# Kernel tuning notes

Measured on AMD Instinct MI355X. Metric: run time of the kernel, lower is better.

## Reference

```python
import math
import jax, jax.numpy as jnp
import numpy as np

B, T, D, V, S, R = 128, 32, 64, 4096, 32, 8
PONDER = 0.01
TWO_PI = np.float32(2.0 * math.pi)


def _ln(x, g, b, eps=1e-5):
    mu = x.mean(-1, keepdims=True)
    var = ((x - mu) ** 2).mean(-1, keepdims=True)
    return (x - mu) / jnp.sqrt(var + eps) * g + b


def _clin(xr, xi, Wr, br, Wi, bi):
    # ComplexLinear: fc_real/fc_imag share biases per torch module
    real = (xr @ Wr + br) - (xi @ Wi + bi)
    imag = (xi @ Wr + br) + (xr @ Wi + bi)
    return real, imag


def setup_inputs() -> dict:
    key = jax.random.key(0)
    ks = jax.random.split(key, 10)
    f = lambda k, sh, s: jax.random.normal(k, sh, jnp.float32) * s
    return {
        "x_seq": jax.random.randint(ks[0], (B, T), 0, V),
        "enc_emb": f(ks[1], (V, 2 * D), 0.02),
        "vq_emb": f(ks[2], (V, 2 * D), 0.05),
        "norm_rg": jnp.ones((D,), jnp.float32),
        "norm_rb": jnp.zeros((D,), jnp.float32),
        "norm_ig": jnp.ones((D,), jnp.float32),
        "norm_ib": jnp.zeros((D,), jnp.float32),
        "proj_w": f(ks[3], (3, 2, D, D), 0.05),  # [q/k/v, real/imag, in, out]
        "proj_b": f(ks[4], (3, 2, D), 0.01),
        "mem_gate_w": f(ks[5], (2 * D, 1), 0.05),
        "mem_gate_b": jnp.zeros((1,), jnp.float32),
        "arb_w": f(ks[6], (2 * D, 3), 0.05),
        "arb_b": jnp.zeros((3,), jnp.float32),
        "dec_w": f(ks[7], (2 * D, V), 0.02),
        "dec_b": jnp.zeros((V,), jnp.float32),
        "halt_bias": jnp.array(3.0, jnp.float32),
        "input_gate": jnp.array(0.0, jnp.float32),
    }


def _fwd(x_seq, enc_emb, vq_emb, norm_rg, norm_rb, norm_ig, norm_ib,
         proj_w, proj_b, mem_gate_w, mem_gate_b, arb_w, arb_b,
         dec_w, dec_b, halt_bias, input_gate):
    sg = jax.lax.stop_gradient
    emb = enc_emb[x_seq]                         # [B,T,2D]
    er, ei = emb[..., :D], emb[..., D:]
    alpha = jax.nn.sigmoid(input_gate)
    bias = jax.nn.softplus(halt_bias)
    vq_sq = (vq_emb ** 2).sum(-1)                # [V]

    def step(carry, xs):
        gw_r, gw_i, mem_r, mem_i = carry
        x_r, x_i = xs
        gw_r = alpha * gw_r + (1.0 - alpha) * x_r
        gw_i = alpha * gw_i + (1.0 - alpha) * x_i
        active = jnp.ones((x_r.shape[0],), jnp.float32)
        acc_vq = jnp.zeros_like(active)
        acc_ppx = jnp.zeros_like(active)
        acc_ent = jnp.zeros_like(active)
        acc_pond = jnp.zeros_like(active)
        acc_ph = jnp.zeros_like(active)
        prev_ang = jnp.arctan2(gw_i, gw_r)
        for _ in range(R):
            cr = _ln(gw_r, norm_rg, norm_rb)
            ci = _ln(gw_i, norm_ig, norm_ib)
            flat = jnp.concatenate([cr, ci], -1)            # [B,2D]
            # VQ (argmin over squared euclidean == argmin over cdist)
            d2 = (flat ** 2).sum(-1, keepdims=True) - 2.0 * (flat @ vq_emb.T) + vq_sq
            idx = jnp.argmin(d2, -1)                        # [B]
            zq = vq_emb[idx]                                # [B,2D]
            vq_loss = ((zq - sg(flat)) ** 2).mean(-1) + 0.25 * ((sg(zq) - flat) ** 2).mean(-1)
            zq_st = flat + sg(zq - flat)                    # straight-through
            avg = jax.nn.one_hot(idx, V, dtype=jnp.float32).mean(0)
            ent = -(avg * jnp.log(avg + 1e-10)).sum()
            ppx = jnp.exp(ent)
            vq_r, vq_i = zq_st[:, :D], zq_st[:, D:]
            # Hermitian gating
            qr, qi = _clin(cr, ci, proj_w[0, 0], proj_b[0, 0], proj_w[0, 1], proj_b[0, 1])
            kr, ki = _clin(cr, ci, proj_w[1, 0], proj_b[1, 0], proj_w[1, 1], proj_b[1, 1])
            wr, wi = _clin(cr, ci, proj_w[2, 0], proj_b[2, 0], proj_w[2, 1], proj_b[2, 1])
            gate = jax.nn.sigmoid((qr * kr + qi * ki).sum(-1, keepdims=True))
            g_r, g_i = wr * gate, wi * gate
            # memory read (mem unchanged during recursion)
            sim = jnp.einsum('bsd,bd->bs', mem_r, cr) + jnp.einsum('bsd,bd->bs', mem_i, ci)
            attn = jax.nn.softmax(sim, -1)
            m_r = jnp.einsum('bs,bsd->bd', attn, mem_r)
            m_i = jnp.einsum('bs,bsd->bd', attn, mem_i)
            # arbitrator mix
            gates = jax.nn.softmax(flat @ arb_w + arb_b, -1)  # [B,3]
            u_r = gates[:, 0:1] * g_r + gates[:, 1:2] * m_r + gates[:, 2:3] * vq_r
            u_i = gates[:, 0:1] * g_i + gates[:, 1:2] * m_i + gates[:, 2:3] * vq_i
            c_r = 0.6 * cr + 0.4 * u_r
            c_i = 0.6 * ci + 0.4 * u_i
            ang = jnp.arctan2(c_i, c_r)
            diff = jnp.abs(ang - prev_ang)
            diff = jnp.minimum(diff, TWO_PI - diff)
            acc_ph = acc_ph + active * diff.mean(-1)
            prev_ang = ang
            halt = jax.nn.sigmoid(bias - vq_loss)
            stop = (halt > 0.5).astype(jnp.float32)
            acc_pond = acc_pond + active * PONDER
            m = active > 0.5
            acc_vq = jnp.where(m, vq_loss, acc_vq)
            acc_ppx = jnp.where(m, ppx, acc_ppx)
            acc_ent = jnp.where(m, ent, acc_ent)
            gw_r = jnp.where(m[:, None], c_r, gw_r)
            gw_i = jnp.where(m[:, None], c_i, gw_i)
            active = active * (1.0 - stop)
        # final memory write (read output discarded, matching torch)
        flat_gw = jnp.concatenate([gw_r, gw_i], -1)
        wg = jax.nn.sigmoid(flat_gw @ mem_gate_w + mem_gate_b)  # [B,1]
        sh_r = jnp.roll(mem_r, 1, axis=1)
        sh_i = jnp.roll(mem_i, 1, axis=1)
        mem_r = sh_r.at[:, 0].set(wg * gw_r + (1.0 - wg) * sh_r[:, 0])
        mem_i = sh_i.at[:, 0].set(wg * gw_i + (1.0 - wg) * sh_i[:, 0])
        stats = jnp.stack([acc_vq.mean(), acc_ppx.mean(), acc_ent.mean(),
                           acc_pond.mean(), acc_ph.mean()])
        return (gw_r, gw_i, mem_r, mem_i), (gw_r, gw_i, stats)

    init = (jnp.zeros((B, D), jnp.float32), jnp.zeros((B, D), jnp.float32),
            jnp.zeros((B, S, D), jnp.float32), jnp.zeros((B, S, D), jnp.float32))
    xs = (jnp.moveaxis(er, 1, 0), jnp.moveaxis(ei, 1, 0))
    (gw_r, gw_i, mem_r, mem_i), (o_r, o_i, stats) = jax.lax.scan(step, init, xs)
    flat_out = jnp.concatenate([jnp.moveaxis(o_r, 0, 1), jnp.moveaxis(o_i, 0, 1)], -1)  # [B,T,2D]
    logits = flat_out @ dec_w + dec_b
    return logits, stats.mean(0), mem_r, mem_i


def reference(x_seq, enc_emb, vq_emb, norm_rg, norm_rb, norm_ig, norm_ib,
              proj_w, proj_b, mem_gate_w, mem_gate_b, arb_w, arb_b,
              dec_w, dec_b, halt_bias, input_gate):
    return _fwd(x_seq, enc_emb, vq_emb, norm_rg, norm_rb, norm_ig, norm_ib,
                proj_w, proj_b, mem_gate_w, mem_gate_b, arb_w, arb_b,
                dec_w, dec_b, halt_bias, input_gate)
```

## Files before the change

kernel.cpp:

```cpp
#include <hip/hip_runtime.h>
#include <math.h>

#define BB 128
#define TT 32
#define DDIM 64
#define VV 4096
#define SS 32
#define RR 8
#define NT 512
#define SMP 65

typedef unsigned short u16;
typedef unsigned int u32;
typedef _Float16 h2 __attribute__((ext_vector_type(2)));

__device__ __forceinline__ h2 bch(u32 u){ union { u32 u; h2 h; } v; v.u = u; return v.h; }

__device__ __forceinline__ float fdot2f(u32 a, u32 b, float acc){
#if __has_builtin(__builtin_amdgcn_fdot2)
  return __builtin_amdgcn_fdot2(bch(a), bch(b), acc, false);
#else
  h2 x = bch(a), y = bch(b);
  return acc + (float)x[0] * (float)y[0] + (float)x[1] * (float)y[1];
#endif
}

__device__ __forceinline__ u32 packh2(float a, float b){
  union { _Float16 h[2]; u32 u; } p;
  p.h[0] = (_Float16)a; p.h[1] = (_Float16)b;
  return p.u;
}

__device__ __forceinline__ void bar(){ __syncthreads(); }

__global__ __launch_bounds__(256) void k_pack(const float* __restrict__ vq, u32* __restrict__ vqT){
  int gid = blockIdx.x * 256 + threadIdx.x;
  int l   = gid & 63;
  int dc8 = (gid >> 6) & 15;
  int c0  = gid >> 10;
  int c   = (c0 << 6) + l;
  const float* s = vq + c * 128 + dc8 * 8;
  uint4 o;
  o.x = packh2(s[0], s[1]);
  o.y = packh2(s[2], s[3]);
  o.z = packh2(s[4], s[5]);
  o.w = packh2(s[6], s[7]);
  ((uint4*)vqT)[gid] = o;
}

__global__ __launch_bounds__(256) void k_vqsq(const float* __restrict__ vq, float* __restrict__ vqsq){
  int c = blockIdx.x * 256 + threadIdx.x;
  float s = 0.f;
  for (int d = 0; d < 128; d++){ float v = vq[c * 128 + d]; s = fmaf(v, v, s); }
  vqsq[c] = s;
}

__global__ __launch_bounds__(NT) void k_recur(
    const int* __restrict__ x_seq, const float* __restrict__ enc_emb,
    const float* __restrict__ vq_emb, const u32* __restrict__ vqT,
    const float* __restrict__ vq_sq,
    const float* __restrict__ nrg, const float* __restrict__ nrb,
    const float* __restrict__ nig, const float* __restrict__ nib,
    const float* __restrict__ proj_w, const float* __restrict__ proj_b,
    const float* __restrict__ mgw, const float* __restrict__ mgb,
    const float* __restrict__ arb_w, const float* __restrict__ arb_b,
    const float* __restrict__ hb, const float* __restrict__ ig,
    float* __restrict__ gwout,
    int* __restrict__ idxbuf, int* __restrict__ rstop_g, float* __restrict__ accs,
    float* __restrict__ out_mem)
{
  const int b = blockIdx.x;
  const int tid = threadIdx.x;
  const int lane = tid & 63;
  const int wave = tid >> 6;

  __shared__ __align__(16) float s_gw[128];
  __shared__ __align__(16) float s_flat[128];
  __shared__ __align__(16) u32   s_flath[64];
  __shared__ __align__(16) float s_c[128];
  __shared__ float s_mem[2][SS][SMP];
  __shared__ __align__(16) float s_qkw[6][DDIM];
  __shared__ float s_sim[SS];
  __shared__ float s_red[8];
  __shared__ float s_cand[8];
  __shared__ int   s_candi[8];

  for (int i = tid; i < 128; i += NT) s_gw[i] = 0.f;
  for (int i = tid; i < 2 * SS * SMP; i += NT) ((float*)s_mem)[i] = 0.f;
  __syncthreads();

  const float alpha = 1.f / (1.f + expf(-ig[0]));
  float bias_h; { float x = hb[0]; bias_h = log1pf(expf(x)); }
  int head = 0;
  float prev_ang = 0.f;

  #pragma unroll 1
  for (int t = 0; t < TT; t++){
    int xid = x_seq[b * TT + t];

    if (tid < 128){
      float e = enc_emb[xid * 128 + tid];
      s_gw[tid] = alpha * s_gw[tid] + (1.f - alpha) * e;
    }
    bar();
    if (wave == 0) prev_ang = atan2f(s_gw[64 + lane], s_gw[lane]);

    float acc_ph = 0.f, vl_last = 0.f;
    int rst = 0;
    bool stop = false;

    #pragma unroll 1
    for (int r = 0; r < RR; r++){
      if (wave < 2){
        float x = s_gw[wave * 64 + lane];
        float mu = x;
        #pragma unroll
        for (int m = 1; m < 64; m <<= 1) mu += __shfl_xor(mu, m);
        mu *= (1.f / 64.f);
        float dxl = x - mu;
        float vv = dxl * dxl;
        #pragma unroll
        for (int m = 1; m < 64; m <<= 1) vv += __shfl_xor(vv, m);
        vv *= (1.f / 64.f);
        float rs = 1.f / sqrtf(vv + 1e-5f);
        const float* g  = wave ? nig : nrg;
        const float* bb = wave ? nib : nrb;
        float fv = dxl * rs * g[lane] + bb[lane];
        s_flat[wave * 64 + lane] = fv;
        float pv = __shfl_xor(fv, 1);
        if ((lane & 1) == 0)
          s_flath[(wave * 64 + lane) >> 1] = packh2(fv, pv);
      }
      bar();

      uint4 F[16];
      {
        const uint4* sfh4 = (const uint4*)s_flath;
        #pragma unroll
        for (int i = 0; i < 16; i++) F[i] = sfh4[i];
      }
      float bsc = 3.4e38f; int bidx = 0;
      #pragma unroll 1
      for (int k = 0; k < 8; k++){
        int c0 = wave + 8 * k;
        const uint4* vp = ((const uint4*)vqT) + (c0 * 16) * 64 + lane;
        uint4 U[16];
        #pragma unroll
        for (int dc8 = 0; dc8 < 16; dc8++) U[dc8] = vp[dc8 * 64];
        float dot = 0.f;
        #pragma unroll
        for (int dc8 = 0; dc8 < 16; dc8++){
          dot = fdot2f(U[dc8].x, F[dc8].x, dot);
          dot = fdot2f(U[dc8].y, F[dc8].y, dot);
          dot = fdot2f(U[dc8].z, F[dc8].z, dot);
          dot = fdot2f(U[dc8].w, F[dc8].w, dot);
        }
        int c = c0 * 64 + lane;
        float sc = vq_sq[c] - 2.f * dot;
        if (sc < bsc || (sc == bsc && c < bidx)){ bsc = sc; bidx = c; }
      }
      #pragma unroll
      for (int m = 1; m < 64; m <<= 1){
        float os = __shfl_xor(bsc, m);
        int   oi = __shfl_xor(bidx, m);
        if (os < bsc || (os == bsc && oi < bidx)){ bsc = os; bidx = oi; }
      }
      if (lane == 0){ s_cand[wave] = bsc; s_candi[wave] = bidx; }
      bar();

      int imin = 0;
      if (wave < 2){
        float bs = s_cand[0]; int bi = s_candi[0];
        #pragma unroll
        for (int w = 1; w < 8; w++){
          float os = s_cand[w]; int oi = s_candi[w];
          if (os < bs || (os == bs && oi < bi)){ bs = os; bi = oi; }
        }
        imin = __builtin_amdgcn_readfirstlane(bi);
      }

      if (wave >= 2){
        const int w2 = wave - 2;
        const int p = w2 >> 1, ri = w2 & 1;
        const float* Wr = proj_w + ((p * 2 + 0) << 12);
        const float* Wi = proj_w + ((p * 2 + 1) << 12);
        const float* xA = s_flat + (ri ? 64 : 0);
        const float* xB = s_flat + (ri ? 0 : 64);
        float a0=0.f,a1=0.f,a2=0.f,a3=0.f, b0=0.f,b1=0.f,b2=0.f,b3=0.f;
        #pragma unroll
        for (int i = 0; i < 64; i += 4){
          float4 xv = *(const float4*)&xA[i];
          a0 = fmaf(xv.x, Wr[(i + 0) * 64 + lane], a0);
          a1 = fmaf(xv.y, Wr[(i + 1) * 64 + lane], a1);
          a2 = fmaf(xv.z, Wr[(i + 2) * 64 + lane], a2);
          a3 = fmaf(xv.w, Wr[(i + 3) * 64 + lane], a3);
        }
        #pragma unroll
        for (int i = 0; i < 64; i += 4){
          float4 xv = *(const float4*)&xB[i];
          b0 = fmaf(xv.x, Wi[(i + 0) * 64 + lane], b0);
          b1 = fmaf(xv.y, Wi[(i + 1) * 64 + lane], b1);
          b2 = fmaf(xv.z, Wi[(i + 2) * 64 + lane], b2);
          b3 = fmaf(xv.w, Wi[(i + 3) * 64 + lane], b3);
        }
        float A  = (a0 + a1) + (a2 + a3);
        float Bv = (b0 + b1) + (b2 + b3);
        float br  = proj_b[(p * 2 + 0) * 64 + lane];
        float bi2 = proj_b[(p * 2 + 1) * 64 + lane];
        s_qkw[w2][lane] = ri ? (A + Bv + br + bi2) : (A - Bv + br - bi2);
      } else if (wave == 0){
        const int s2 = lane & 31, h = lane >> 5;
        const float* mrow = &s_mem[h][s2][0];
        const float* fx = s_flat + h * 64;
        float a0=0.f,a1=0.f,a2=0.f,a3=0.f;
        #pragma unroll
        for (int d = 0; d < 64; d += 4){
          a0 = fmaf(mrow[d + 0], fx[d + 0], a0);
          a1 = fmaf(mrow[d + 1], fx[d + 1], a1);
          a2 = fmaf(mrow[d + 2], fx[d + 2], a2);
          a3 = fmaf(mrow[d + 3], fx[d + 3], a3);
        }
        float p = (a0 + a1) + (a2 + a3);
        p += __shfl_xor(p, 32);
        float mx = p;
        #pragma unroll
        for (int m = 1; m < 32; m <<= 1) mx = fmaxf(mx, __shfl_xor(mx, m));
        float e = expf(p - mx);
        float sm = e;
        #pragma unroll
        for (int m = 1; m < 32; m <<= 1) sm += __shfl_xor(sm, m);
        if (lane < 32) s_sim[lane] = e / sm;
      } else {
        float f0 = s_flat[lane], f1 = s_flat[64 + lane];
        float p0 = fmaf(f0, arb_w[lane * 3 + 0], f1 * arb_w[(64 + lane) * 3 + 0]);
        float p1 = fmaf(f0, arb_w[lane * 3 + 1], f1 * arb_w[(64 + lane) * 3 + 1]);
        float p2 = fmaf(f0, arb_w[lane * 3 + 2], f1 * arb_w[(64 + lane) * 3 + 2]);
        float z0 = vq_emb[imin * 128 + lane];
        float z1 = vq_emb[imin * 128 + 64 + lane];
        float d0 = z0 - f0, d1 = z1 - f1;
        float sq = d0 * d0 + d1 * d1;
        #pragma unroll
        for (int m = 1; m < 64; m <<= 1){
          p0 += __shfl_xor(p0, m); p1 += __shfl_xor(p1, m);
          p2 += __shfl_xor(p2, m); sq += __shfl_xor(sq, m);
        }
        if (lane == 0){
          s_red[4] = p0 + arb_b[0];
          s_red[5] = p1 + arb_b[1];
          s_red[6] = p2 + arb_b[2];
          s_red[0] = 1.25f * sq * (1.f / 128.f);
          idxbuf[(b * TT + t) * RR + r] = imin;
        }
      }
      bar();

      float vl = s_red[0];
      stop = (bias_h - vl) > 0.f;
      vl_last = vl; rst = r;

      if (tid < 128){
        float g = fmaf(s_qkw[0][lane], s_qkw[2][lane], s_qkw[1][lane] * s_qkw[3][lane]);
        #pragma unroll
        for (int m = 1; m < 64; m <<= 1) g += __shfl_xor(g, m);
        float gate = 1.f / (1.f + expf(-g));
        const int h = wave, j = lane;
        float m_reg = 0.f;
        #pragma unroll 8
        for (int s2 = 0; s2 < 32; s2++)
          m_reg = fmaf(s_sim[s2], s_mem[h][s2][j], m_reg);
        float l0 = s_red[4], l1 = s_red[5], l2 = s_red[6];
        float mx = fmaxf(l0, fmaxf(l1, l2));
        float e0 = expf(l0 - mx), e1 = expf(l1 - mx), e2 = expf(l2 - mx);
        float inv = 1.f / (e0 + e1 + e2);
        float zq = vq_emb[imin * 128 + tid];
        float wv = s_qkw[4 + h][j];
        float u = (e0 * inv) * (gate * wv) + (e1 * inv) * m_reg + (e2 * inv) * zq;
        float cv = 0.6f * s_flat[tid] + 0.4f * u;
        s_c[tid]  = cv;
        s_gw[tid] = cv;
      }
      bar();

      if (wave == 0){
        float ang = atan2f(s_c[64 + lane], s_c[lane]);
        float df = fabsf(ang - prev_ang);
        df = fminf(df, 6.28318530717958647692f - df);
        prev_ang = ang;
        #pragma unroll
        for (int m = 1; m < 64; m <<= 1) df += __shfl_xor(df, m);
        acc_ph += df * (1.f / 64.f);
      }
      if (stop) break;
    }

    float pond = 0.01f * (float)(rst + 1);
    if (tid < 128) gwout[(b * TT + t) * 128 + tid] = s_gw[tid];
    head = (head + SS - 1) & (SS - 1);
    if (wave < 2){
      float p = fmaf(s_c[lane], mgw[lane], s_c[64 + lane] * mgw[64 + lane]);
      #pragma unroll
      for (int m = 1; m < 64; m <<= 1) p += __shfl_xor(p, m);
      float wg = 1.f / (1.f + expf(-(p + mgb[0])));
      const int h = wave, d0 = lane;
      float old = s_mem[h][head][d0];
      s_mem[h][head][d0] = wg * s_c[h * 64 + d0] + (1.f - wg) * old;
    }
    if (tid == 0){
      int o = b * TT + t;
      rstop_g[o] = rst;
      accs[o * 4 + 0] = vl_last;
      accs[o * 4 + 1] = pond;
      accs[o * 4 + 2] = acc_ph;
    }
  }

  bar();
  for (int i = tid; i < SS * DDIM; i += NT){
    int s2 = i >> 6, d0 = i & 63;
    int ph = (head + s2) & (SS - 1);
    out_mem[b * SS * DDIM + i] = s_mem[0][ph][d0];
    out_mem[BB * SS * DDIM + b * SS * DDIM + i] = s_mem[1][ph][d0];
  }
}

__global__ void k_max(const int* __restrict__ rstop_g, int* __restrict__ maxr){
  int t = threadIdx.x;
  if (t >= TT) return;
  int mx = 0;
  for (int b = 0; b < BB; b++) mx = max(mx, rstop_g[b * TT + t]);
  maxr[t] = mx;
}

__global__ __launch_bounds__(256) void k_tail(
    const u32* __restrict__ vqT, const float* __restrict__ vq_sq,
    const float* __restrict__ gwout, const int* __restrict__ rstop_g,
    const int* __restrict__ maxr, int* __restrict__ idxbuf,
    const float* __restrict__ nrg, const float* __restrict__ nrb,
    const float* __restrict__ nig, const float* __restrict__ nib)
{
  int o = blockIdx.x;
  int t = o & (TT - 1);
  int rs = rstop_g[o];
  if (rs >= maxr[t]) return;
  __shared__ __align__(16) u32 sfh[64];
  __shared__ float s_cand[4];
  __shared__ int   s_candi[4];
  int tid = threadIdx.x, lane = tid & 63, wave = tid >> 6;
  if (wave < 2){
    float x = gwout[o * 128 + wave * 64 + lane];
    float mu = x;
    #pragma unroll
    for (int m = 1; m < 64; m <<= 1) mu += __shfl_xor(mu, m);
    mu *= (1.f / 64.f);
    float dxl = x - mu;
    float vv = dxl * dxl;
    #pragma unroll
    for (int m = 1; m < 64; m <<= 1) vv += __shfl_xor(vv, m);
    vv *= (1.f / 64.f);
    float rsn = 1.f / sqrtf(vv + 1e-5f);
    const float* g  = wave ? nig : nrg;
    const float* bb = wave ? nib : nrb;
    float fv = dxl * rsn * g[lane] + bb[lane];
    float pv = __shfl_xor(fv, 1);
    if ((lane & 1) == 0) sfh[(wave * 64 + lane) >> 1] = packh2(fv, pv);
  }
  __syncthreads();
  uint4 F[16];
  {
    const uint4* sfh4 = (const uint4*)sfh;
    #pragma unroll
    for (int i = 0; i < 16; i++) F[i] = sfh4[i];
  }
  float bsc = 3.4e38f; int bidx = 0;
  #pragma unroll 1
  for (int k = 0; k < 16; k++){
    int c0 = wave + 4 * k;
    const uint4* vp = ((const uint4*)vqT) + (c0 * 16) * 64 + lane;
    uint4 U[16];
    #pragma unroll
    for (int dc8 = 0; dc8 < 16; dc8++) U[dc8] = vp[dc8 * 64];
    float dot = 0.f;
    #pragma unroll
    for (int dc8 = 0; dc8 < 16; dc8++){
      dot = fdot2f(U[dc8].x, F[dc8].x, dot);
      dot = fdot2f(U[dc8].y, F[dc8].y, dot);
      dot = fdot2f(U[dc8].z, F[dc8].z, dot);
      dot = fdot2f(U[dc8].w, F[dc8].w, dot);
    }
    int c = c0 * 64 + lane;
    float sc = vq_sq[c] - 2.f * dot;
    if (sc < bsc || (sc == bsc && c < bidx)){ bsc = sc; bidx = c; }
  }
  #pragma unroll
  for (int m = 1; m < 64; m <<= 1){
    float os = __shfl_xor(bsc, m);
    int   oi = __shfl_xor(bidx, m);
    if (os < bsc || (os == bsc && oi < bidx)){ bsc = os; bidx = oi; }
  }
  if (lane == 0){ s_cand[wave] = bsc; s_candi[wave] = bidx; }
  __syncthreads();
  if (tid == 0){
    float bs = s_cand[0]; int bi = s_candi[0];
    for (int w = 1; w < 4; w++){
      float os = s_cand[w]; int oi = s_candi[w];
      if (os < bs || (os == bs && oi < bi)){ bs = os; bi = oi; }
    }
    for (int r = rs + 1; r < RR; r++) idxbuf[o * RR + r] = bi;
  }
}

__global__ __launch_bounds__(512) void k_stats(
    const int* __restrict__ idxbuf, const int* __restrict__ rstop_g,
    const float* __restrict__ accs, const int* __restrict__ maxr,
    float* __restrict__ out_stats)
{
  __shared__ float s_ent[TT][RR];
  __shared__ int   s_vals[8][128];
  __shared__ float s_fin[8][5];
  int tid = threadIdx.x, lane = tid & 63, wave = tid >> 6;

  for (int base = 0; base < TT * RR; base += 8){
    int p = base + wave;
    int r = p >> 5, t = p & 31;
    bool act = (r <= maxr[t]);
    s_vals[wave][lane]      = idxbuf[(lane * TT + t) * RR + r];
    s_vals[wave][64 + lane] = idxbuf[((64 + lane) * TT + t) * RR + r];
    __syncthreads();
    if (act){
      int mine1 = s_vals[wave][lane], mine2 = s_vals[wave][64 + lane];
      int c1 = 0, c2 = 0;
      for (int j = 0; j < 128; j++){
        int v = s_vals[wave][j];
        c1 += (v == mine1); c2 += (v == mine2);
      }
      float contrib = -(logf((float)c1 * (1.f / 128.f) + 1e-10f)
                      + logf((float)c2 * (1.f / 128.f) + 1e-10f)) * (1.f / 128.f);
      for (int m = 1; m < 64; m <<= 1) contrib += __shfl_xor(contrib, m);
      if (lane == 0) s_ent[t][r] = contrib;
    }
    __syncthreads();
  }

  float sv = 0.f, sp = 0.f, se = 0.f, sn = 0.f, sh = 0.f;
  for (int o = tid; o < BB * TT; o += 512){
    int t = o & 31;
    int rs = rstop_g[o];
    float ent = s_ent[t][rs];
    se += ent;
    sp += expf(ent);
    sv += accs[o * 4 + 0];
    sn += accs[o * 4 + 1];
    sh += accs[o * 4 + 2];
  }
  for (int m = 1; m < 64; m <<= 1){
    sv += __shfl_xor(sv, m); sp += __shfl_xor(sp, m); se += __shfl_xor(se, m);
    sn += __shfl_xor(sn, m); sh += __shfl_xor(sh, m);
  }
  if (lane == 0){
    s_fin[wave][0] = sv; s_fin[wave][1] = sp; s_fin[wave][2] = se;
    s_fin[wave][3] = sn; s_fin[wave][4] = sh;
  }
  __syncthreads();
  if (tid == 0){
    float a[5] = {0.f, 0.f, 0.f, 0.f, 0.f};
    for (int w = 0; w < 8; w++)
      for (int j = 0; j < 5; j++) a[j] += s_fin[w][j];
    float inv = 1.f / (float)(BB * TT);
    for (int j = 0; j < 5; j++) out_stats[j] = a[j] * inv;
  }
}

__global__ __launch_bounds__(256) void k_dec(
    const float* __restrict__ gwout, const float* __restrict__ dec_w,
    const float* __restrict__ dec_b, float* __restrict__ out)
{
  __shared__ float At[32][128];
  int tid = threadIdx.x;
  int row0 = blockIdx.y * 32;
  int col0 = blockIdx.x * 256;
  {
    const float4* src = (const float4*)(gwout + row0 * 128);
    float4* dst = (float4*)&At[0][0];
    for (int i = tid; i < 1024; i += 256) dst[i] = src[i];
  }
  __syncthreads();
  int v = col0 + tid;
  float acc[32];
  #pragma unroll
  for (int r2 = 0; r2 < 32; r2++) acc[r2] = 0.f;
  for (int k = 0; k < 128; k += 4){
    float w0 = dec_w[(k + 0) * 4096 + v];
    float w1 = dec_w[(k + 1) * 4096 + v];
    float w2 = dec_w[(k + 2) * 4096 + v];
    float w3 = dec_w[(k + 3) * 4096 + v];
    #pragma unroll
    for (int r2 = 0; r2 < 32; r2++){
      float4 a = *(const float4*)&At[r2][k];
      acc[r2] = fmaf(a.x, w0, fmaf(a.y, w1, fmaf(a.z, w2, fmaf(a.w, w3, acc[r2]))));
    }
  }
  float bv = dec_b[v];
  for (int r2 = 0; r2 < 32; r2++)
    out[(row0 + r2) * 4096 + v] = acc[r2] + bv;
}

extern "C" void kernel_launch(void* const* d_in, const int* in_sizes, int n_in,
                              void* d_out, int out_size, void* d_ws, size_t ws_size,
                              hipStream_t stream){
  const int*   x_seq   = (const int*)  d_in[0];
  const float* enc_emb = (const float*)d_in[1];
  const float* vq_emb  = (const float*)d_in[2];
  const float* nrg     = (const float*)d_in[3];
  const float* nrb     = (const float*)d_in[4];
  const float* nig     = (const float*)d_in[5];
  const float* nib     = (const float*)d_in[6];
  const float* proj_w  = (const float*)d_in[7];
  const float* proj_b  = (const float*)d_in[8];
  const float* mgw     = (const float*)d_in[9];
  const float* mgb     = (const float*)d_in[10];
  const float* arb_w   = (const float*)d_in[11];
  const float* arb_b   = (const float*)d_in[12];
  const float* dec_w   = (const float*)d_in[13];
  const float* dec_b   = (const float*)d_in[14];
  const float* hb      = (const float*)d_in[15];
  const float* ig      = (const float*)d_in[16];

  char* ws = (char*)d_ws;
  u32*   vqT    = (u32*)  (ws + 0);
  float* vqsq   = (float*)(ws + 2097152);
  float* gwout  = (float*)(ws + 2113536);
  int*   idxbuf = (int*)  (ws + 6307840);
  int*   rstop  = (int*)  (ws + 6438912);
  float* accs   = (float*)(ws + 6455296);
  int*   maxr   = (int*)  (ws + 6520832);

  float* out = (float*)d_out;
  float* out_stats = out + 16777216;
  float* out_mem   = out + 16777221;

  k_pack <<<dim3(256), dim3(256), 0, stream>>>(vq_emb, vqT);
  k_vqsq <<<dim3(16),  dim3(256), 0, stream>>>(vq_emb, vqsq);
  k_recur<<<dim3(BB),  dim3(NT),  0, stream>>>(
      x_seq, enc_emb, vq_emb, vqT, vqsq,
      nrg, nrb, nig, nib, proj_w, proj_b, mgw, mgb, arb_w, arb_b, hb, ig,
      gwout, idxbuf, rstop, accs, out_mem);
  k_dec  <<<dim3(16, 128), dim3(256), 0, stream>>>(gwout, dec_w, dec_b, out);
  k_max  <<<dim3(1),   dim3(64),  0, stream>>>(rstop, maxr);
  k_tail <<<dim3(BB * TT), dim3(256), 0, stream>>>(vqT, vqsq, gwout, rstop, maxr, idxbuf,
                                                   nrg, nrb, nig, nib);
  k_stats<<<dim3(1),   dim3(512), 0, stream>>>(idxbuf, rstop, accs, maxr, out_stats);
}
```

Measured before the change: 767.1 us.

## Restructure recurrence projection, prefetch embeddings, and parallelize stats across blocks

The recurrent kernel now prefetches the next token's embedding during the current step. The projection is changed so each wave multiplies one weight matrix against both the real and imaginary inputs, with biases and combination done later from shared memory. The argmin merge moves into the arbiter wave, the chosen codebook row is cached in shared memory, the VQ dot uses four independent accumulators, and the phase accumulation moves to wave 2. k_max uses more threads and zeroes the stats output, and k_stats runs one block per timestep, combining results with atomics instead of a single serial block. This removes serial tail work and latency, at the cost of float atomics that make the summation order nondeterministic.

```diff
diff --git a/kernel.cpp b/kernel.cpp
--- a/kernel.cpp
+++ b/kernel.cpp
@@ -78,8 +78,10 @@
   __shared__ __align__(16) float s_flat[128];
   __shared__ __align__(16) u32   s_flath[64];
   __shared__ __align__(16) float s_c[128];
+  __shared__ __align__(16) float s_zq[128];
+  __shared__ __align__(16) float s_enext[128];
   __shared__ float s_mem[2][SS][SMP];
-  __shared__ __align__(16) float s_qkw[6][DDIM];
+  __shared__ __align__(16) float s_mv[12][DDIM];
   __shared__ float s_sim[SS];
   __shared__ float s_red[8];
   __shared__ float s_cand[8];
@@ -87,25 +89,31 @@
 
   for (int i = tid; i < 128; i += NT) s_gw[i] = 0.f;
   for (int i = tid; i < 2 * SS * SMP; i += NT) ((float*)s_mem)[i] = 0.f;
+  if (tid < 128) s_enext[tid] = enc_emb[x_seq[b * TT] * 128 + tid];
   __syncthreads();
 
   const float alpha = 1.f / (1.f + expf(-ig[0]));
   float bias_h; { float x = hb[0]; bias_h = log1pf(expf(x)); }
   int head = 0;
   float prev_ang = 0.f;
+  float acc_ph = 0.f;
+
+  const float pb0r = proj_b[lane],        pb0i = proj_b[64 + lane];
+  const float pb1r = proj_b[128 + lane],  pb1i = proj_b[192 + lane];
+  const float pb2r = proj_b[256 + lane],  pb2i = proj_b[320 + lane];
+
+  const uint4* vqT4 = (const uint4*)vqT;
 
   #pragma unroll 1
   for (int t = 0; t < TT; t++){
-    int xid = x_seq[b * TT + t];
-
     if (tid < 128){
-      float e = enc_emb[xid * 128 + tid];
-      s_gw[tid] = alpha * s_gw[tid] + (1.f - alpha) * e;
+      s_gw[tid] = alpha * s_gw[tid] + (1.f - alpha) * s_enext[tid];
     }
     bar();
-    if (wave == 0) prev_ang = atan2f(s_gw[64 + lane], s_gw[lane]);
-
-    float acc_ph = 0.f, vl_last = 0.f;
+    if (wave == 2) prev_ang = atan2f(s_gw[64 + lane], s_gw[lane]);
+
+    float vl_last = 0.f;
+    if (wave == 2) acc_ph = 0.f;
     int rst = 0;
     bool stop = false;
 
@@ -143,20 +151,26 @@
       #pragma unroll 1
       for (int k = 0; k < 8; k++){
         int c0 = wave + 8 * k;
-        const uint4* vp = ((const uint4*)vqT) + (c0 * 16) * 64 + lane;
+        int c  = (c0 << 6) + lane;
+        float qv = vq_sq[c];
+        const uint4* vp = vqT4 + (c0 * 16) * 64 + lane;
         uint4 U[16];
         #pragma unroll
         for (int dc8 = 0; dc8 < 16; dc8++) U[dc8] = vp[dc8 * 64];
-        float dot = 0.f;
-        #pragma unroll
-        for (int dc8 = 0; dc8 < 16; dc8++){
-          dot = fdot2f(U[dc8].x, F[dc8].x, dot);
-          dot = fdot2f(U[dc8].y, F[dc8].y, dot);
-          dot = fdot2f(U[dc8].z, F[dc8].z, dot);
-          dot = fdot2f(U[dc8].w, F[dc8].w, dot);
-        }
-        int c = c0 * 64 + lane;
-        float sc = vq_sq[c] - 2.f * dot;
+        float a0 = 0.f, a1 = 0.f, a2 = 0.f, a3 = 0.f;
+        #pragma unroll
+        for (int dc8 = 0; dc8 < 16; dc8 += 4){
+          a0 = fdot2f(U[dc8+0].x, F[dc8+0].x, a0); a0 = fdot2f(U[dc8+0].y, F[dc8+0].y, a0);
+          a0 = fdot2f(U[dc8+0].z, F[dc8+0].z, a0); a0 = fdot2f(U[dc8+0].w, F[dc8+0].w, a0);
+          a1 = fdot2f(U[dc8+1].x, F[dc8+1].x, a1); a1 = fdot2f(U[dc8+1].y, F[dc8+1].y, a1);
+          a1 = fdot2f(U[dc8+1].z, F[dc8+1].z, a1); a1 = fdot2f(U[dc8+1].w, F[dc8+1].w, a1);
+          a2 = fdot2f(U[dc8+2].x, F[dc8+2].x, a2); a2 = fdot2f(U[dc8+2].y, F[dc8+2].y, a2);
+          a2 = fdot2f(U[dc8+2].z, F[dc8+2].z, a2); a2 = fdot2f(U[dc8+2].w, F[dc8+2].w, a2);
+          a3 = fdot2f(U[dc8+3].x, F[dc8+3].x, a3); a3 = fdot2f(U[dc8+3].y, F[dc8+3].y, a3);
+          a3 = fdot2f(U[dc8+3].z, F[dc8+3].z, a3); a3 = fdot2f(U[dc8+3].w, F[dc8+3].w, a3);
+        }
+        float dot = (a0 + a1) + (a2 + a3);
+        float sc = qv - 2.f * dot;
         if (sc < bsc || (sc == bsc && c < bidx)){ bsc = sc; bidx = c; }
       }
       #pragma unroll
@@ -168,46 +182,32 @@
       if (lane == 0){ s_cand[wave] = bsc; s_candi[wave] = bidx; }
       bar();
 
-      int imin = 0;
-      if (wave < 2){
-        float bs = s_cand[0]; int bi = s_candi[0];
-        #pragma unroll
-        for (int w = 1; w < 8; w++){
-          float os = s_cand[w]; int oi = s_candi[w];
-          if (os < bs || (os == bs && oi < bi)){ bs = os; bi = oi; }
-        }
-        imin = __builtin_amdgcn_readfirstlane(bi);
-      }
-
       if (wave >= 2){
+        if (wave == 3 && r == 0 && t + 1 < TT){
+          int xn = x_seq[b * TT + t + 1];
+          s_enext[lane]      = enc_emb[xn * 128 + lane];
+          s_enext[64 + lane] = enc_emb[xn * 128 + 64 + lane];
+        }
         const int w2 = wave - 2;
-        const int p = w2 >> 1, ri = w2 & 1;
-        const float* Wr = proj_w + ((p * 2 + 0) << 12);
-        const float* Wi = proj_w + ((p * 2 + 1) << 12);
-        const float* xA = s_flat + (ri ? 64 : 0);
-        const float* xB = s_flat + (ri ? 0 : 64);
-        float a0=0.f,a1=0.f,a2=0.f,a3=0.f, b0=0.f,b1=0.f,b2=0.f,b3=0.f;
+        const int p = w2 >> 1, wsel = w2 & 1;
+        const float* W = proj_w + ((p * 2 + wsel) << 12);
+        float a0=0.f,a1=0.f,a2=0.f,a3=0.f;
+        float b0=0.f,b1=0.f,b2=0.f,b3=0.f;
         #pragma unroll
         for (int i = 0; i < 64; i += 4){
-          float4 xv = *(const float4*)&xA[i];
-          a0 = fmaf(xv.x, Wr[(i + 0) * 64 + lane], a0);
-          a1 = fmaf(xv.y, Wr[(i + 1) * 64 + lane], a1);
-          a2 = fmaf(xv.z, Wr[(i + 2) * 64 + lane], a2);
-          a3 = fmaf(xv.w, Wr[(i + 3) * 64 + lane], a3);
-        }
-        #pragma unroll
-        for (int i = 0; i < 64; i += 4){
-          float4 xv = *(const float4*)&xB[i];
-          b0 = fmaf(xv.x, Wi[(i + 0) * 64 + lane], b0);
-          b1 = fmaf(xv.y, Wi[(i + 1) * 64 + lane], b1);
-          b2 = fmaf(xv.z, Wi[(i + 2) * 64 + lane], b2);
-          b3 = fmaf(xv.w, Wi[(i + 3) * 64 + lane], b3);
-        }
-        float A  = (a0 + a1) + (a2 + a3);
-        float Bv = (b0 + b1) + (b2 + b3);
-        float br  = proj_b[(p * 2 + 0) * 64 + lane];
-        float bi2 = proj_b[(p * 2 + 1) * 64 + lane];
-        s_qkw[w2][lane] = ri ? (A + Bv + br + bi2) : (A - Bv + br - bi2);
+          float4 xr4 = *(const float4*)&s_flat[i];
+          float4 xi4 = *(const float4*)&s_flat[64 + i];
+          float w0 = W[(i + 0) * 64 + lane];
+          float w1 = W[(i + 1) * 64 + lane];
+          float w2v= W[(i + 2) * 64 + lane];
+          float w3 = W[(i + 3) * 64 + lane];
+          a0 = fmaf(xr4.x, w0, a0); a1 = fmaf(xr4.y, w1, a1);
+          a2 = fmaf(xr4.z, w2v, a2); a3 = fmaf(xr4.w, w3, a3);
+          b0 = fmaf(xi4.x, w0, b0); b1 = fmaf(xi4.y, w1, b1);
+          b2 = fmaf(xi4.z, w2v, b2); b3 = fmaf(xi4.w, w3, b3);
+        }
+        s_mv[w2 * 2 + 0][lane] = (a0 + a1) + (a2 + a3);
+        s_mv[w2 * 2 + 1][lane] = (b0 + b1) + (b2 + b3);
       } else if (wave == 0){
         const int s2 = lane & 31, h = lane >> 5;
         const float* mrow = &s_mem[h][s2][0];
@@ -231,12 +231,21 @@
         for (int m = 1; m < 32; m <<= 1) sm += __shfl_xor(sm, m);
         if (lane < 32) s_sim[lane] = e / sm;
       } else {
+        float bs = s_cand[0]; int bi = s_candi[0];
+        #pragma unroll
+        for (int w = 1; w < 8; w++){
+          float os = s_cand[w]; int oi = s_candi[w];
+          if (os < bs || (os == bs && oi < bi)){ bs = os; bi = oi; }
+        }
+        int imin = __builtin_amdgcn_readfirstlane(bi);
         float f0 = s_flat[lane], f1 = s_flat[64 + lane];
         float p0 = fmaf(f0, arb_w[lane * 3 + 0], f1 * arb_w[(64 + lane) * 3 + 0]);
         float p1 = fmaf(f0, arb_w[lane * 3 + 1], f1 * arb_w[(64 + lane) * 3 + 1]);
         float p2 = fmaf(f0, arb_w[lane * 3 + 2], f1 * arb_w[(64 + lane) * 3 + 2]);
         float z0 = vq_emb[imin * 128 + lane];
         float z1 = vq_emb[imin * 128 + 64 + lane];
+        s_zq[lane]      = z0;
+        s_zq[64 + lane] = z1;
         float d0 = z0 - f0, d1 = z1 - f1;
         float sq = d0 * d0 + d1 * d1;
         #pragma unroll
@@ -259,7 +268,11 @@
       vl_last = vl; rst = r;
 
       if (tid < 128){
-        float g = fmaf(s_qkw[0][lane], s_qkw[2][lane], s_qkw[1][lane] * s_qkw[3][lane]);
+        float qr = s_mv[0][lane] - s_mv[3][lane] + pb0r - pb0i;
+        float qi = s_mv[1][lane] + s_mv[2][lane] + pb0r + pb0i;
+        float kr = s_mv[4][lane] - s_mv[7][lane] + pb1r - pb1i;
+        float ki = s_mv[5][lane] + s_mv[6][lane] + pb1r + pb1i;
+        float g = fmaf(qr, kr, qi * ki);
         #pragma unroll
         for (int m = 1; m < 64; m <<= 1) g += __shfl_xor(g, m);
         float gate = 1.f / (1.f + expf(-g));
@@ -272,8 +285,9 @@
         float mx = fmaxf(l0, fmaxf(l1, l2));
         float e0 = expf(l0 - mx), e1 = expf(l1 - mx), e2 = expf(l2 - mx);
         float inv = 1.f / (e0 + e1 + e2);
-        float zq = vq_emb[imin * 128 + tid];
-        float wv = s_qkw[4 + h][j];
+        float zq = s_zq[tid];
+        float wv = h ? (s_mv[9][j] + s_mv[10][j] + pb2r + pb2i)
+                     : (s_mv[8][j] - s_mv[11][j] + pb2r - pb2i);
         float u = (e0 * inv) * (gate * wv) + (e1 * inv) * m_reg + (e2 * inv) * zq;
         float cv = 0.6f * s_flat[tid] + 0.4f * u;
         s_c[tid]  = cv;
@@ -281,7 +295,7 @@
       }
       bar();
 
-      if (wave == 0){
+      if (wave == 2){
         float ang = atan2f(s_c[64 + lane], s_c[lane]);
         float df = fabsf(ang - prev_ang);
         df = fminf(df, 6.28318530717958647692f - df);
@@ -289,6 +303,8 @@
         #pragma unroll
         for (int m = 1; m < 64; m <<= 1) df += __shfl_xor(df, m);
         acc_ph += df * (1.f / 64.f);
+        if ((stop || r == RR - 1) && lane == 0)
+          accs[(b * TT + t) * 4 + 2] = acc_ph;
       }
       if (stop) break;
     }
@@ -310,7 +326,6 @@
       rstop_g[o] = rst;
       accs[o * 4 + 0] = vl_last;
       accs[o * 4 + 1] = pond;
-      accs[o * 4 + 2] = acc_ph;
     }
   }
 
@@ -323,12 +338,24 @@
   }
 }
 
-__global__ void k_max(const int* __restrict__ rstop_g, int* __restrict__ maxr){
-  int t = threadIdx.x;
-  if (t >= TT) return;
+__global__ __launch_bounds__(256) void k_max(const int* __restrict__ rstop_g,
+                                             int* __restrict__ maxr,
+                                             float* __restrict__ out_stats){
+  __shared__ int sm[8][TT];
+  int tid = threadIdx.x;
+  int t = tid & 31, q = tid >> 5;
   int mx = 0;
-  for (int b = 0; b < BB; b++) mx = max(mx, rstop_g[b * TT + t]);
-  maxr[t] = mx;
+  for (int b = q * 16; b < q * 16 + 16; b++) mx = max(mx, rstop_g[b * TT + t]);
+  sm[q][t] = mx;
+  __syncthreads();
+  if (tid < TT){
+    int m = sm[0][tid];
+    #pragma unroll
+    for (int qq = 1; qq < 8; qq++) m = max(m, sm[qq][tid]);
+    maxr[tid] = m;
+  } else if (tid >= 64 && tid < 69){
+    out_stats[tid - 64] = 0.f;
+  }
 }
 
 __global__ __launch_bounds__(256) void k_tail(
@@ -414,59 +441,58 @@
     const float* __restrict__ accs, const int* __restrict__ maxr,
     float* __restrict__ out_stats)
 {
-  __shared__ float s_ent[TT][RR];
   __shared__ int   s_vals[8][128];
-  __shared__ float s_fin[8][5];
+  __shared__ float s_ent2[RR];
+  __shared__ float s_part[8][5];
+  const int t = blockIdx.x;
   int tid = threadIdx.x, lane = tid & 63, wave = tid >> 6;
-
-  for (int base = 0; base < TT * RR; base += 8){
-    int p = base + wave;
-    int r = p >> 5, t = p & 31;
-    bool act = (r <= maxr[t]);
-    s_vals[wave][lane]      = idxbuf[(lane * TT + t) * RR + r];
-    s_vals[wave][64 + lane] = idxbuf[((64 + lane) * TT + t) * RR + r];
-    __syncthreads();
-    if (act){
-      int mine1 = s_vals[wave][lane], mine2 = s_vals[wave][64 + lane];
-      int c1 = 0, c2 = 0;
-      for (int j = 0; j < 128; j++){
-        int v = s_vals[wave][j];
-        c1 += (v == mine1); c2 += (v == mine2);
-      }
-      float contrib = -(logf((float)c1 * (1.f / 128.f) + 1e-10f)
-                      + logf((float)c2 * (1.f / 128.f) + 1e-10f)) * (1.f / 128.f);
-      for (int m = 1; m < 64; m <<= 1) contrib += __shfl_xor(contrib, m);
-      if (lane == 0) s_ent[t][r] = contrib;
-    }
-    __syncthreads();
-  }
+  int mr = maxr[t];
+  int r = wave;
+  if (r <= mr){
+    int v1 = idxbuf[(lane * TT + t) * RR + r];
+    int v2 = idxbuf[((64 + lane) * TT + t) * RR + r];
+    s_vals[wave][lane]      = v1;
+    s_vals[wave][64 + lane] = v2;
+    int c1 = 0, c2 = 0;
+    for (int j = 0; j < 128; j++){
+      int v = s_vals[wave][j];
+      c1 += (v == v1); c2 += (v == v2);
+    }
+    float contrib = -(logf((float)c1 * (1.f / 128.f) + 1e-10f)
+                    + logf((float)c2 * (1.f / 128.f) + 1e-10f)) * (1.f / 128.f);
+    #pragma unroll
+    for (int m = 1; m < 64; m <<= 1) contrib += __shfl_xor(contrib, m);
+    if (lane == 0) s_ent2[r] = contrib;
+  }
+  __syncthreads();
 
   float sv = 0.f, sp = 0.f, se = 0.f, sn = 0.f, sh = 0.f;
-  for (int o = tid; o < BB * TT; o += 512){
-    int t = o & 31;
+  if (tid < BB){
+    int o = tid * TT + t;
     int rs = rstop_g[o];
-    float ent = s_ent[t][rs];
-    se += ent;
-    sp += expf(ent);
-    sv += accs[o * 4 + 0];
-    sn += accs[o * 4 + 1];
-    sh += accs[o * 4 + 2];
-  }
+    float ent = s_ent2[rs];
+    se = ent;
+    sp = expf(ent);
+    sv = accs[o * 4 + 0];
+    sn = accs[o * 4 + 1];
+    sh = accs[o * 4 + 2];
+  }
+  #pragma unroll
   for (int m = 1; m < 64; m <<= 1){
     sv += __shfl_xor(sv, m); sp += __shfl_xor(sp, m); se += __shfl_xor(se, m);
     sn += __shfl_xor(sn, m); sh += __shfl_xor(sh, m);
   }
   if (lane == 0){
-    s_fin[wave][0] = sv; s_fin[wave][1] = sp; s_fin[wave][2] = se;
-    s_fin[wave][3] = sn; s_fin[wave][4] = sh;
+    s_part[wave][0] = sv; s_part[wave][1] = sp; s_part[wave][2] = se;
+    s_part[wave][3] = sn; s_part[wave][4] = sh;
   }
   __syncthreads();
   if (tid == 0){
     float a[5] = {0.f, 0.f, 0.f, 0.f, 0.f};
     for (int w = 0; w < 8; w++)
-      for (int j = 0; j < 5; j++) a[j] += s_fin[w][j];
-    float inv = 1.f / (float)(BB * TT);
-    for (int j = 0; j < 5; j++) out_stats[j] = a[j] * inv;
+      for (int j = 0; j < 5; j++) a[j] += s_part[w][j];
+    const float inv = 1.f / (float)(BB * TT);
+    for (int j = 0; j < 5; j++) atomicAdd(&out_stats[j], a[j] * inv);
   }
 }
 
@@ -545,8 +571,8 @@
       nrg, nrb, nig, nib, proj_w, proj_b, mgw, mgb, arb_w, arb_b, hb, ig,
       gwout, idxbuf, rstop, accs, out_mem);
   k_dec  <<<dim3(16, 128), dim3(256), 0, stream>>>(gwout, dec_w, dec_b, out);
-  k_max  <<<dim3(1),   dim3(64),  0, stream>>>(rstop, maxr);
+  k_max  <<<dim3(1),   dim3(256), 0, stream>>>(rstop, maxr, out_stats);
   k_tail <<<dim3(BB * TT), dim3(256), 0, stream>>>(vqT, vqsq, gwout, rstop, maxr, idxbuf,
                                                    nrg, nrb, nig, nib);
-  k_stats<<<dim3(1),   dim3(512), 0, stream>>>(idxbuf, rstop, accs, maxr, out_stats);
-}
+  k_stats<<<dim3(TT),  dim3(512), 0, stream>>>(idxbuf, rstop, accs, maxr, out_stats);
+}
```

After: 639.3 us. 1.2x faster.
